# Performance work log

Hardware: AMD Instinct MI355X
Metric: run time of the kernel (lower is better)

Reference implementation:

```python
import jax, jax.numpy as jnp
import numpy as np

B, T, D = 32, 512, 1024   # batch, seq_len, input_dim
H, L, O = 1024, 4, 1024   # hidden_dim, num_layers, output_dim


def setup_inputs() -> dict:
    key = jax.random.key(0)
    ks = jax.random.split(key, 8)
    s_in = 1.0 / np.sqrt(D)
    s_h = 1.0 / np.sqrt(H)
    # Weights stored as [in, out]; y = x @ W + b (equivalent to torch Linear with W.T)
    return {
        "x":     jax.random.normal(ks[0], (B, T, D), dtype=jnp.float32),
        "W_in":  jax.random.uniform(ks[1], (L, D, H), minval=-s_in, maxval=s_in, dtype=jnp.float32),
        "b_in":  jax.random.uniform(ks[2], (L, H),    minval=-s_in, maxval=s_in, dtype=jnp.float32),
        "W_h":   jax.random.uniform(ks[3], (L, H, H), minval=-s_h,  maxval=s_h,  dtype=jnp.float32),
        "b_h":   jax.random.uniform(ks[4], (L, H),    minval=-s_h,  maxval=s_h,  dtype=jnp.float32),
        "tau":   jnp.ones((L, H), dtype=jnp.float32),
        "W_out": jax.random.uniform(ks[5], (H, O),    minval=-s_h,  maxval=s_h,  dtype=jnp.float32),
        "b_out": jax.random.uniform(ks[6], (O,),      minval=-s_h,  maxval=s_h,  dtype=jnp.float32),
    }


def reference(x, W_in, b_in, W_h, b_h, tau, W_out, b_out):
    n_layers = W_in.shape[0]

    def step(h, x_t):
        # h: [L, B, H]; x_t: [B, D]
        xt = x_t
        new_h = []
        for i in range(n_layers):
            dx = jnp.tanh(xt @ W_in[i] + b_in[i] + h[i] @ W_h[i] + b_h[i])
            hi = h[i] + (dx - h[i]) / tau[i]
            new_h.append(hi)
            xt = hi
        return jnp.stack(new_h), None

    h0 = jnp.zeros((n_layers, x.shape[0], W_h.shape[-1]), dtype=x.dtype)
    hT, _ = jax.lax.scan(step, h0, jnp.swapaxes(x, 0, 1))  # scan over time axis
    return hT[-1] @ W_out + b_out  # [B, O]
```

## Files before the change

### kernel.cpp

```cpp
#include <hip/hip_runtime.h>
#include <math.h>

#define B_ 32
#define T_ 512
#define D_ 1024
#define H_ 1024
#define L_ 4
#define NTICK (T_ + L_ - 1)
#define RPD 17
#define PACK_PER_BLK 32768

typedef unsigned long long u64;

__device__ __forceinline__ float4 load_state4(const float* p) {
    u64 a = __hip_atomic_load((const u64*)p,       __ATOMIC_RELAXED, __HIP_MEMORY_SCOPE_AGENT);
    u64 b = __hip_atomic_load((const u64*)(p + 2), __ATOMIC_RELAXED, __HIP_MEMORY_SCOPE_AGENT);
    float4 v;
    v.x = __uint_as_float((unsigned)(a & 0xffffffffu));
    v.y = __uint_as_float((unsigned)(a >> 32));
    v.z = __uint_as_float((unsigned)(b & 0xffffffffu));
    v.w = __uint_as_float((unsigned)(b >> 32));
    return v;
}

__device__ __forceinline__ void waitCount(const unsigned int* p, unsigned int target) {
    int c = 0;
    while (__hip_atomic_load(p, __ATOMIC_RELAXED, __HIP_MEMORY_SCOPE_AGENT) < target) {
        __builtin_amdgcn_s_sleep(16);
        if (++c > 20000) return;
    }
}

__global__ __launch_bounds__(512) void lnn_repack(
    const float* __restrict__ W_in, const float* __restrict__ W_h,
    float* __restrict__ Wpack)
{
    const int bid   = blockIdx.x;
    const int layer = bid >> 6;
    const int jbase = (bid & 63) << 4;
    const float* Win_l = W_in + (size_t)layer * D_ * H_;
    const float* Wh_l  = W_h  + (size_t)layer * H_ * H_;
    float* dst = Wpack + (size_t)bid * PACK_PER_BLK;
#pragma unroll 1
    for (int i = 0; i < 16; ++i) {
        const int f  = (i << 9) + threadIdx.x;
        const int d  = f << 2;
        const int jj = d >> 11;
        const int k  = d & 2047;
        const float* s = (k < 1024) ? &Win_l[(size_t)k * H_ + jbase + jj]
                                    : &Wh_l[(size_t)(k - 1024) * H_ + jbase + jj];
        float4 v;
        v.x = s[0];
        v.y = s[(size_t)H_];
        v.z = s[(size_t)2 * H_];
        v.w = s[(size_t)3 * H_];
        *(float4*)&dst[d] = v;
    }
}

#define REDUCE_PHASE(P)                                                         \
    do {                                                                        \
        __syncthreads();                                                        \
        _Pragma("unroll")                                                       \
        for (int q = 0; q < 8; ++q) {                                           \
            red[tid * RPD + (q << 1)]     = acc[((P) << 3) + q].x;              \
            red[tid * RPD + (q << 1) + 1] = acc[((P) << 3) + q].y;              \
        }                                                                       \
        __syncthreads();                                                        \
        if (tid < 128) {                                                        \
            const int bo   = tid >> 4;                                          \
            const int bh   = ((P) << 3) + bo;                                   \
            const int js   = (tid & 15) >> 1;                                   \
            const int comp = tid & 1;                                           \
            float s = 0.f;                                                      \
            _Pragma("unroll")                                                   \
            for (int ks = 0; ks < 64; ++ks)                                     \
                s += red[((ks << 3) + js) * RPD + (bo << 1) + comp];            \
            const float dx   = tanhf(s + bias);                                 \
            const float hold = __hip_atomic_load(&hrow[(size_t)bh * H_ + jr],   \
                                __ATOMIC_RELAXED, __HIP_MEMORY_SCOPE_AGENT);    \
            const float hn   = hold + (dx - hold) / tv;                         \
            __hip_atomic_store(&wl[(size_t)bh * H_ + jr], hn,                   \
                               __ATOMIC_RELAXED, __HIP_MEMORY_SCOPE_AGENT);     \
        }                                                                       \
    } while (0)

template<bool PACKED>
__global__ __launch_bounds__(512, 2) void lnn_persist(
    const float* __restrict__ x,
    const float* __restrict__ W_in,
    const float* __restrict__ b_in,
    const float* __restrict__ W_h,
    const float* __restrict__ b_h,
    const float* __restrict__ tau,
    const float* __restrict__ Wpack,
    float* __restrict__ buf0,
    float* __restrict__ buf1,
    unsigned int* __restrict__ count)
{
    const int tid   = threadIdx.x;
    const int layer = blockIdx.x >> 6;
    const int jbase = (blockIdx.x & 63) << 4;
    const int jp    = tid & 7;
    const int kslot = tid >> 3;
    const int kb    = kslot << 2;

    __shared__ __align__(16) float smem[16384];
    float (*xs)[32][256] = (float(*)[32][256])smem;
    float* red = smem;

    const float* Wl_in = W_in + (size_t)layer * D_ * H_;
    const float* Wl_h  = W_h  + (size_t)layer * H_ * H_;
    const float* wbaseA = Wpack + (size_t)blockIdx.x * PACK_PER_BLK
                        + ((size_t)(jp << 1) << 11);
    const float* wbaseB = wbaseA + 2048;
    const int jgA = jbase + (jp << 1);

    const int   jr   = jbase + (tid & 15);
    const float bias = b_in[layer * H_ + jr] + b_h[layer * H_ + jr];
    const float tv   = tau[layer * H_ + jr];

    const int srow = tid >> 6;
    const int scol = (tid & 63) << 2;

    for (int tick = 0; tick < NTICK; ++tick) {
        if (tid == 0 && tick > 0)
            waitCount(&count[tick - 1], 256u);
        __syncthreads();

        const int t = tick - layer;
        if (t >= 0 && t < T_) {
            const float* rb   = (tick & 1) ? buf0 : buf1;
            float*       wb   = (tick & 1) ? buf1 : buf0;
            const float* hrow = rb + (size_t)layer * B_ * H_;
            float*       wl   = wb + (size_t)layer * B_ * H_;

            const float* xsrc; size_t xstr;
            if (layer == 0) { xsrc = x + (size_t)t * D_;                  xstr = (size_t)T_ * D_; }
            else            { xsrc = rb + (size_t)(layer - 1) * B_ * H_;  xstr = H_; }

            float2 acc[32];
#pragma unroll
            for (int i = 0; i < 32; ++i) acc[i] = make_float2(0.f, 0.f);

            {
                const bool at0 = (layer != 0);
#pragma unroll
                for (int q = 0; q < 4; ++q) {
                    const int r = srow + (q << 3);
                    const float* sp = &xsrc[(size_t)r * xstr + scol];
                    float4 v = at0 ? load_state4(sp) : *(const float4*)sp;
                    *(float4*)&xs[0][r][scol] = v;
                }
            }
            __syncthreads();

#pragma unroll 1
            for (int tile = 0; tile < 8; ++tile) {
                const int cur = tile & 1;

                float4 wA, wB;
                if constexpr (PACKED) {
                    wA = *(const float4*)&wbaseA[(tile << 8) + kb];
                    wB = *(const float4*)&wbaseB[(tile << 8) + kb];
                } else {
                    const int kof = (tile & 3) << 8;
                    const float* wp = ((tile < 4) ? Wl_in : Wl_h)
                                    + (size_t)(kof + kb) * H_ + jgA;
                    wA.x = wp[0];            wB.x = wp[1];
                    wA.y = wp[(size_t)H_];   wB.y = wp[(size_t)H_ + 1];
                    wA.z = wp[2*(size_t)H_]; wB.z = wp[2*(size_t)H_ + 1];
                    wA.w = wp[3*(size_t)H_]; wB.w = wp[3*(size_t)H_ + 1];
                }

                float4 stg[4];
                if (tile < 7) {
                    const int    nt   = tile + 1;
                    const float* nsrc = (nt < 4) ? xsrc : hrow;
                    const size_t nstr = (nt < 4) ? xstr : (size_t)H_;
                    const int    nkof = (nt & 3) << 8;
                    const bool   nat  = (nt >= 4) || (layer != 0);
#pragma unroll
                    for (int q = 0; q < 4; ++q) {
                        const int r = srow + (q << 3);
                        const float* sp = &nsrc[(size_t)r * nstr + nkof + scol];
                        stg[q] = nat ? load_state4(sp) : *(const float4*)sp;
                    }
                }

#pragma unroll
                for (int b = 0; b < 32; ++b) {
                    const float4 a = *(const float4*)&xs[cur][b][kb];
                    acc[b].x += a.x * wA.x + a.y * wA.y + a.z * wA.z + a.w * wA.w;
                    acc[b].y += a.x * wB.x + a.y * wB.y + a.z * wB.z + a.w * wB.w;
                }

                if (tile < 7) {
#pragma unroll
                    for (int q = 0; q < 4; ++q)
                        *(float4*)&xs[cur ^ 1][srow + (q << 3)][scol] = stg[q];
                }
                __syncthreads();
            }

            REDUCE_PHASE(0); REDUCE_PHASE(1); REDUCE_PHASE(2); REDUCE_PHASE(3);
        }

        __syncthreads();
        if (tid == 0)
            __hip_atomic_fetch_add(&count[tick], 1u,
                                   __ATOMIC_RELEASE, __HIP_MEMORY_SCOPE_AGENT);
    }
}

__global__ __launch_bounds__(256) void lnn_out(
    const float* __restrict__ H3,
    const float* __restrict__ W_out,
    const float* __restrict__ b_out,
    float* __restrict__ out)
{
    const int gid = blockIdx.x * 256 + threadIdx.x;
    const int jj  = gid & 1023;
    const int b2  = gid >> 10;
    float acc0 = b_out[jj];
    float acc1 = b_out[jj];
    for (int k = 0; k < H_; ++k) {
        const float w = W_out[k * H_ + jj];
        acc0 += H3[b2 * H_ + k]        * w;
        acc1 += H3[(b2 + 16) * H_ + k] * w;
    }
    out[b2 * H_ + jj]        = acc0;
    out[(b2 + 16) * H_ + jj] = acc1;
}

extern "C" void kernel_launch(void* const* d_in, const int* in_sizes, int n_in,
                              void* d_out, int out_size, void* d_ws, size_t ws_size,
                              hipStream_t stream) {
    const float* x     = (const float*)d_in[0];
    const float* W_in  = (const float*)d_in[1];
    const float* b_in  = (const float*)d_in[2];
    const float* W_h   = (const float*)d_in[3];
    const float* b_h   = (const float*)d_in[4];
    const float* tau   = (const float*)d_in[5];
    const float* W_out = (const float*)d_in[6];
    const float* b_out = (const float*)d_in[7];

    const size_t stateElems = (size_t)L_ * B_ * H_;
    const size_t packElems  = (size_t)256 * PACK_PER_BLK;
    const size_t needPacked = (packElems + 2 * stateElems) * sizeof(float)
                            + NTICK * sizeof(unsigned int);
    const bool packed = (ws_size >= needPacked);

    float* Wpack = (float*)d_ws;
    float* buf0  = packed ? (Wpack + packElems) : (float*)d_ws;
    float* buf1  = buf0 + stateElems;
    unsigned int* count = (unsigned int*)(buf1 + stateElems);

    (void)hipMemsetAsync(buf0, 0,
                         2 * stateElems * sizeof(float) + NTICK * sizeof(unsigned int), stream);

    if (packed) {
        lnn_repack<<<256, 512, 0, stream>>>(W_in, W_h, Wpack);
        lnn_persist<true><<<256, 512, 0, stream>>>(x, W_in, b_in, W_h, b_h, tau,
                                                   Wpack, buf0, buf1, count);
    } else {
        lnn_persist<false><<<256, 512, 0, stream>>>(x, W_in, b_in, W_h, b_h, tau,
                                                    Wpack, buf0, buf1, count);
    }

    const float* H3 = buf0 + 3 * (B_ * H_);
    lnn_out<<<64, 256, 0, stream>>>(H3, W_out, b_out, (float*)d_out);
}
```

Baseline: 15.54 ms.

## Shard tick counters and stage two K-tiles per barrier in persistent RNN

The single per-tick arrival counter becomes 8 padded sub-counters. Each block increments the one chosen by its block index, and the waiter sums all 8, so the 256 atomic adds no longer hit one address. Shared memory doubles to hold two 256-wide K-tiles per buffer half, so the inner loop handles tiles in pairs and issues half as many __syncthreads per timestep. The trade-offs are 128KB of LDS per block, which rules out the two-blocks-per-CU occupancy the launch bounds ask for, and a waiter that must poll 8 cache lines per tick.

Result: no change. 15.71 ms (+1.1%).

```diff
diff --git a/kernel.cpp b/kernel.cpp
--- a/kernel.cpp
+++ b/kernel.cpp
@@ -9,6 +9,8 @@
 #define NTICK (T_ + L_ - 1)
 #define RPD 17
 #define PACK_PER_BLK 32768
+#define CNT_STRIDE 16
+#define CNT_PER_TICK (8 * CNT_STRIDE)
 
 typedef unsigned long long u64;
 
@@ -23,9 +25,15 @@
     return v;
 }
 
-__device__ __forceinline__ void waitCount(const unsigned int* p, unsigned int target) {
+__device__ __forceinline__ void waitTick(const unsigned int* base) {
     int c = 0;
-    while (__hip_atomic_load(p, __ATOMIC_RELAXED, __HIP_MEMORY_SCOPE_AGENT) < target) {
+    for (;;) {
+        unsigned s = 0;
+#pragma unroll
+        for (int i = 0; i < 8; ++i)
+            s += __hip_atomic_load(base + i * CNT_STRIDE,
+                                   __ATOMIC_RELAXED, __HIP_MEMORY_SCOPE_AGENT);
+        if (s >= 256u) return;
         __builtin_amdgcn_s_sleep(16);
         if (++c > 20000) return;
     }
@@ -85,6 +93,25 @@
         }                                                                       \
     } while (0)
 
+#define STAGE_TILE(TSRC, TSTR, TKOF, TAT, DSTPTR)                               \
+    do {                                                                        \
+        float4 stg0, stg1, stg2, stg3;                                          \
+        {                                                                       \
+            const float* sp0 = &(TSRC)[(size_t)(srow)      * (TSTR) + (TKOF) + scol]; \
+            const float* sp1 = &(TSRC)[(size_t)(srow + 8)  * (TSTR) + (TKOF) + scol]; \
+            const float* sp2 = &(TSRC)[(size_t)(srow + 16) * (TSTR) + (TKOF) + scol]; \
+            const float* sp3 = &(TSRC)[(size_t)(srow + 24) * (TSTR) + (TKOF) + scol]; \
+            if (TAT) { stg0 = load_state4(sp0); stg1 = load_state4(sp1);        \
+                       stg2 = load_state4(sp2); stg3 = load_state4(sp3); }      \
+            else     { stg0 = *(const float4*)sp0; stg1 = *(const float4*)sp1;  \
+                       stg2 = *(const float4*)sp2; stg3 = *(const float4*)sp3; }\
+        }                                                                       \
+        *(float4*)&(DSTPTR)[(size_t)(srow)      * 256 + scol] = stg0;           \
+        *(float4*)&(DSTPTR)[(size_t)(srow + 8)  * 256 + scol] = stg1;           \
+        *(float4*)&(DSTPTR)[(size_t)(srow + 16) * 256 + scol] = stg2;           \
+        *(float4*)&(DSTPTR)[(size_t)(srow + 24) * 256 + scol] = stg3;           \
+    } while (0)
+
 template<bool PACKED>
 __global__ __launch_bounds__(512, 2) void lnn_persist(
     const float* __restrict__ x,
@@ -105,8 +132,7 @@
     const int kslot = tid >> 3;
     const int kb    = kslot << 2;
 
-    __shared__ __align__(16) float smem[16384];
-    float (*xs)[32][256] = (float(*)[32][256])smem;
+    __shared__ __align__(16) float smem[32768];
     float* red = smem;
 
     const float* Wl_in = W_in + (size_t)layer * D_ * H_;
@@ -125,7 +151,7 @@
 
     for (int tick = 0; tick < NTICK; ++tick) {
         if (tid == 0 && tick > 0)
-            waitCount(&count[tick - 1], 256u);
+            waitTick(count + (size_t)(tick - 1) * CNT_PER_TICK);
         __syncthreads();
 
         const int t = tick - layer;
@@ -138,68 +164,83 @@
             const float* xsrc; size_t xstr;
             if (layer == 0) { xsrc = x + (size_t)t * D_;                  xstr = (size_t)T_ * D_; }
             else            { xsrc = rb + (size_t)(layer - 1) * B_ * H_;  xstr = H_; }
+            const bool xat = (layer != 0);
 
             float2 acc[32];
 #pragma unroll
             for (int i = 0; i < 32; ++i) acc[i] = make_float2(0.f, 0.f);
 
-            {
-                const bool at0 = (layer != 0);
+            STAGE_TILE(xsrc, xstr, 0,   xat, smem);
+            STAGE_TILE(xsrc, xstr, 256, xat, smem + 8192);
+            __syncthreads();
+
+#pragma unroll 1
+            for (int p = 0; p < 4; ++p) {
+                const int    bufo = (p & 1) << 14;
+                const int    nbo  = ((p & 1) ^ 1) << 14;
+                const float* cs0  = smem + bufo;
+                const float* cs1  = smem + bufo + 8192;
+                const int ta = (p << 1);
+                const int tb = ta + 1;
+
+                {
+                    float4 wA, wB;
+                    if constexpr (PACKED) {
+                        wA = *(const float4*)&wbaseA[(ta << 8) + kb];
+                        wB = *(const float4*)&wbaseB[(ta << 8) + kb];
+                    } else {
+                        const float* wp = ((ta < 4) ? Wl_in : Wl_h)
+                                        + (size_t)(((ta & 3) << 8) + kb) * H_ + jgA;
+                        wA.x = wp[0];            wB.x = wp[1];
+                        wA.y = wp[(size_t)H_];   wB.y = wp[(size_t)H_ + 1];
+                        wA.z = wp[2*(size_t)H_]; wB.z = wp[2*(size_t)H_ + 1];
+                        wA.w = wp[3*(size_t)H_]; wB.w = wp[3*(size_t)H_ + 1];
+                    }
+                    if (p < 3) {
+                        const int    nt   = ta + 2;
+                        const float* nsrc = (nt < 4) ? xsrc : hrow;
+                        const size_t nstr = (nt < 4) ? xstr : (size_t)H_;
+                        const int    nkof = (nt & 3) << 8;
+                        const bool   nat  = (nt >= 4) || xat;
+                        STAGE_TILE(nsrc, nstr, nkof, nat, smem + nbo);
+                    }
 #pragma unroll
-                for (int q = 0; q < 4; ++q) {
-                    const int r = srow + (q << 3);
-                    const float* sp = &xsrc[(size_t)r * xstr + scol];
-                    float4 v = at0 ? load_state4(sp) : *(const float4*)sp;
-                    *(float4*)&xs[0][r][scol] = v;
+                    for (int b = 0; b < 32; ++b) {
+                        const float4 a = *(const float4*)&cs0[(size_t)b * 256 + kb];
+                        acc[b].x += a.x * wA.x + a.y * wA.y + a.z * wA.z + a.w * wA.w;
+                        acc[b].y += a.x * wB.x + a.y * wB.y + a.z * wB.z + a.w * wB.w;
+                    }
                 }
-            }
-            __syncthreads();
-
-#pragma unroll 1
-            for (int tile = 0; tile < 8; ++tile) {
-                const int cur = tile & 1;
-
-                float4 wA, wB;
-                if constexpr (PACKED) {
-                    wA = *(const float4*)&wbaseA[(tile << 8) + kb];
-                    wB = *(const float4*)&wbaseB[(tile << 8) + kb];
-                } else {
-                    const int kof = (tile & 3) << 8;
-                    const float* wp = ((tile < 4) ? Wl_in : Wl_h)
-                                    + (size_t)(kof + kb) * H_ + jgA;
-                    wA.x = wp[0];            wB.x = wp[1];
-                    wA.y = wp[(size_t)H_];   wB.y = wp[(size_t)H_ + 1];
-                    wA.z = wp[2*(size_t)H_]; wB.z = wp[2*(size_t)H_ + 1];
-                    wA.w = wp[3*(size_t)H_]; wB.w = wp[3*(size_t)H_ + 1];
+
+                {
+                    float4 wA, wB;
+                    if constexpr (PACKED) {
+                        wA = *(const float4*)&wbaseA[(tb << 8) + kb];
+                        wB = *(const float4*)&wbaseB[(tb << 8) + kb];
+                    } else {
+                        const float* wp = ((tb < 4) ? Wl_in : Wl_h)
+                                        + (size_t)(((tb & 3) << 8) + kb) * H_ + jgA;
+                        wA.x = wp[0];            wB.x = wp[1];
+                        wA.y = wp[(size_t)H_];   wB.y = wp[(size_t)H_ + 1];
+                        wA.z = wp[2*(size_t)H_]; wB.z = wp[2*(size_t)H_ + 1];
+                        wA.w = wp[3*(size_t)H_]; wB.w = wp[3*(size_t)H_ + 1];
+                    }
+                    if (p < 3) {
+                        const int    nt   = tb + 2;
+                        const float* nsrc = (nt < 4) ? xsrc : hrow;
+                        const size_t nstr = (nt < 4) ? xstr : (size_t)H_;
+                        const int    nkof = (nt & 3) << 8;
+                        const bool   nat  = (nt >= 4) || xat;
+                        STAGE_TILE(nsrc, nstr, nkof, nat, smem + nbo + 8192);
+                    }
+#pragma unroll
+                    for (int b = 0; b < 32; ++b) {
+                        const float4 a = *(const float4*)&cs1[(size_t)b * 256 + kb];
+                        acc[b].x += a.x * wA.x + a.y * wA.y + a.z * wA.z + a.w * wA.w;
+                        acc[b].y += a.x * wB.x + a.y * wB.y + a.z * wB.z + a.w * wB.w;
+                    }
                 }
 
-                float4 stg[4];
-                if (tile < 7) {
-                    const int    nt   = tile + 1;
-                    const float* nsrc = (nt < 4) ? xsrc : hrow;
-                    const size_t nstr = (nt < 4) ? xstr : (size_t)H_;
-                    const int    nkof = (nt & 3) << 8;
-                    const bool   nat  = (nt >= 4) || (layer != 0);
-#pragma unroll
-                    for (int q = 0; q < 4; ++q) {
-                        const int r = srow + (q << 3);
-                        const float* sp = &nsrc[(size_t)r * nstr + nkof + scol];
-                        stg[q] = nat ? load_state4(sp) : *(const float4*)sp;
-                    }
-                }
-
-#pragma unroll
-                for (int b = 0; b < 32; ++b) {
-                    const float4 a = *(const float4*)&xs[cur][b][kb];
-                    acc[b].x += a.x * wA.x + a.y * wA.y + a.z * wA.z + a.w * wA.w;
-                    acc[b].y += a.x * wB.x + a.y * wB.y + a.z * wB.z + a.w * wB.w;
-                }
-
-                if (tile < 7) {
-#pragma unroll
-                    for (int q = 0; q < 4; ++q)
-                        *(float4*)&xs[cur ^ 1][srow + (q << 3)][scol] = stg[q];
-                }
                 __syncthreads();
             }
 
@@ -208,7 +249,8 @@
 
         __syncthreads();
         if (tid == 0)
-            __hip_atomic_fetch_add(&count[tick], 1u,
+            __hip_atomic_fetch_add(count + (size_t)tick * CNT_PER_TICK
+                                         + (blockIdx.x & 7) * CNT_STRIDE, 1u,
                                    __ATOMIC_RELEASE, __HIP_MEMORY_SCOPE_AGENT);
     }
 }
@@ -247,8 +289,9 @@
 
     const size_t stateElems = (size_t)L_ * B_ * H_;
     const size_t packElems  = (size_t)256 * PACK_PER_BLK;
+    const size_t cntDwords  = (size_t)NTICK * CNT_PER_TICK;
     const size_t needPacked = (packElems + 2 * stateElems) * sizeof(float)
-                            + NTICK * sizeof(unsigned int);
+                            + cntDwords * sizeof(unsigned int);
     const bool packed = (ws_size >= needPacked);
 
     float* Wpack = (float*)d_ws;
@@ -257,7 +300,8 @@
     unsigned int* count = (unsigned int*)(buf1 + stateElems);
 
     (void)hipMemsetAsync(buf0, 0,
-                         2 * stateElems * sizeof(float) + NTICK * sizeof(unsigned int), stream);
+                         2 * stateElems * sizeof(float) + cntDwords * sizeof(unsigned int),
+                         stream);
 
     if (packed) {
         lnn_repack<<<256, 512, 0, stream>>>(W_in, W_h, Wpack);
```

## Replace global per-tick barrier with per-layer dataflow dependency counters

Applied to the files above, without the earlier changes.

Instead of all 256 blocks waiting on a single global counter per tick, each layer's blocks now wait only on their true dependencies: the previous layer at the same timestep, their own layer at the previous timestep, and the next layer two steps back (to protect the double buffer against WAR). This lets layers advance independently as a wavefront and removes the idle tick at the pipeline ends. It adds up to three waits per step and a larger counter array.

Result: faster. 13.31 ms (median of 2 runs) (-14.4%).

```diff
diff --git a/kernel.cpp b/kernel.cpp
--- a/kernel.cpp
+++ b/kernel.cpp
@@ -6,7 +6,6 @@
 #define D_ 1024
 #define H_ 1024
 #define L_ 4
-#define NTICK (T_ + L_ - 1)
 #define RPD 17
 #define PACK_PER_BLK 32768
 
@@ -96,7 +95,7 @@
     const float* __restrict__ Wpack,
     float* __restrict__ buf0,
     float* __restrict__ buf1,
-    unsigned int* __restrict__ count)
+    unsigned int* __restrict__ done)
 {
     const int tid   = threadIdx.x;
     const int layer = blockIdx.x >> 6;
@@ -123,92 +122,93 @@
     const int srow = tid >> 6;
     const int scol = (tid & 63) << 2;
 
-    for (int tick = 0; tick < NTICK; ++tick) {
-        if (tid == 0 && tick > 0)
-            waitCount(&count[tick - 1], 256u);
+    for (int t = 0; t < T_; ++t) {
+        if (tid == 0) {
+            if (layer > 0)             waitCount(&done[(layer - 1) * T_ + t],     64u);
+            if (t >= 1)                waitCount(&done[layer * T_ + (t - 1)],     64u);
+            if (layer < 3 && t >= 2)   waitCount(&done[(layer + 1) * T_ + (t - 2)], 64u);
+        }
         __syncthreads();
 
-        const int t = tick - layer;
-        if (t >= 0 && t < T_) {
-            const float* rb   = (tick & 1) ? buf0 : buf1;
-            float*       wb   = (tick & 1) ? buf1 : buf0;
-            const float* hrow = rb + (size_t)layer * B_ * H_;
-            float*       wl   = wb + (size_t)layer * B_ * H_;
-
-            const float* xsrc; size_t xstr;
-            if (layer == 0) { xsrc = x + (size_t)t * D_;                  xstr = (size_t)T_ * D_; }
-            else            { xsrc = rb + (size_t)(layer - 1) * B_ * H_;  xstr = H_; }
-
-            float2 acc[32];
-#pragma unroll
-            for (int i = 0; i < 32; ++i) acc[i] = make_float2(0.f, 0.f);
-
-            {
-                const bool at0 = (layer != 0);
+        const int par = (t + layer) & 1;
+        const float* rb   = par ? buf0 : buf1;
+        float*       wb   = par ? buf1 : buf0;
+        const float* hrow = rb + (size_t)layer * B_ * H_;
+        float*       wl   = wb + (size_t)layer * B_ * H_;
+
+        const float* xsrc; size_t xstr;
+        if (layer == 0) { xsrc = x + (size_t)t * D_;                  xstr = (size_t)T_ * D_; }
+        else            { xsrc = rb + (size_t)(layer - 1) * B_ * H_;  xstr = H_; }
+
+        float2 acc[32];
+#pragma unroll
+        for (int i = 0; i < 32; ++i) acc[i] = make_float2(0.f, 0.f);
+
+        {
+            const bool at0 = (layer != 0);
+#pragma unroll
+            for (int q = 0; q < 4; ++q) {
+                const int r = srow + (q << 3);
+                const float* sp = &xsrc[(size_t)r * xstr + scol];
+                float4 v = at0 ? load_state4(sp) : *(const float4*)sp;
+                *(float4*)&xs[0][r][scol] = v;
+            }
+        }
+        __syncthreads();
+
+#pragma unroll 1
+        for (int tile = 0; tile < 8; ++tile) {
+            const int cur = tile & 1;
+
+            float4 wA, wB;
+            if constexpr (PACKED) {
+                wA = *(const float4*)&wbaseA[(tile << 8) + kb];
+                wB = *(const float4*)&wbaseB[(tile << 8) + kb];
+            } else {
+                const int kof = (tile & 3) << 8;
+                const float* wp = ((tile < 4) ? Wl_in : Wl_h)
+                                + (size_t)(kof + kb) * H_ + jgA;
+                wA.x = wp[0];            wB.x = wp[1];
+                wA.y = wp[(size_t)H_];   wB.y = wp[(size_t)H_ + 1];
+                wA.z = wp[2*(size_t)H_]; wB.z = wp[2*(size_t)H_ + 1];
+                wA.w = wp[3*(size_t)H_]; wB.w = wp[3*(size_t)H_ + 1];
+            }
+
+            float4 stg[4];
+            if (tile < 7) {
+                const int    nt   = tile + 1;
+                const float* nsrc = (nt < 4) ? xsrc : hrow;
+                const size_t nstr = (nt < 4) ? xstr : (size_t)H_;
+                const int    nkof = (nt & 3) << 8;
+                const bool   nat  = (nt >= 4) || (layer != 0);
 #pragma unroll
                 for (int q = 0; q < 4; ++q) {
                     const int r = srow + (q << 3);
-                    const float* sp = &xsrc[(size_t)r * xstr + scol];
-                    float4 v = at0 ? load_state4(sp) : *(const float4*)sp;
-                    *(float4*)&xs[0][r][scol] = v;
+                    const float* sp = &nsrc[(size_t)r * nstr + nkof + scol];
+                    stg[q] = nat ? load_state4(sp) : *(const float4*)sp;
                 }
             }
+
+#pragma unroll
+            for (int b = 0; b < 32; ++b) {
+                const float4 a = *(const float4*)&xs[cur][b][kb];
+                acc[b].x += a.x * wA.x + a.y * wA.y + a.z * wA.z + a.w * wA.w;
+                acc[b].y += a.x * wB.x + a.y * wB.y + a.z * wB.z + a.w * wB.w;
+            }
+
+            if (tile < 7) {
+#pragma unroll
+                for (int q = 0; q < 4; ++q)
+                    *(float4*)&xs[cur ^ 1][srow + (q << 3)][scol] = stg[q];
+            }
             __syncthreads();
-
-#pragma unroll 1
-            for (int tile = 0; tile < 8; ++tile) {
-                const int cur = tile & 1;
-
-                float4 wA, wB;
-                if constexpr (PACKED) {
-                    wA = *(const float4*)&wbaseA[(tile << 8) + kb];
-                    wB = *(const float4*)&wbaseB[(tile << 8) + kb];
-                } else {
-                    const int kof = (tile & 3) << 8;
-                    const float* wp = ((tile < 4) ? Wl_in : Wl_h)
-                                    + (size_t)(kof + kb) * H_ + jgA;
-                    wA.x = wp[0];            wB.x = wp[1];
-                    wA.y = wp[(size_t)H_];   wB.y = wp[(size_t)H_ + 1];
-                    wA.z = wp[2*(size_t)H_]; wB.z = wp[2*(size_t)H_ + 1];
-                    wA.w = wp[3*(size_t)H_]; wB.w = wp[3*(size_t)H_ + 1];
-                }
-
-                float4 stg[4];
-                if (tile < 7) {
-                    const int    nt   = tile + 1;
-                    const float* nsrc = (nt < 4) ? xsrc : hrow;
-                    const size_t nstr = (nt < 4) ? xstr : (size_t)H_;
-                    const int    nkof = (nt & 3) << 8;
-                    const bool   nat  = (nt >= 4) || (layer != 0);
-#pragma unroll
-                    for (int q = 0; q < 4; ++q) {
-                        const int r = srow + (q << 3);
-                        const float* sp = &nsrc[(size_t)r * nstr + nkof + scol];
-                        stg[q] = nat ? load_state4(sp) : *(const float4*)sp;
-                    }
-                }
-
-#pragma unroll
-                for (int b = 0; b < 32; ++b) {
-                    const float4 a = *(const float4*)&xs[cur][b][kb];
-                    acc[b].x += a.x * wA.x + a.y * wA.y + a.z * wA.z + a.w * wA.w;
-                    acc[b].y += a.x * wB.x + a.y * wB.y + a.z * wB.z + a.w * wB.w;
-                }
-
-                if (tile < 7) {
-#pragma unroll
-                    for (int q = 0; q < 4; ++q)
-                        *(float4*)&xs[cur ^ 1][srow + (q << 3)][scol] = stg[q];
-                }
-                __syncthreads();
-            }
-
-            REDUCE_PHASE(0); REDUCE_PHASE(1); REDUCE_PHASE(2); REDUCE_PHASE(3);
         }
+
+        REDUCE_PHASE(0); REDUCE_PHASE(1); REDUCE_PHASE(2); REDUCE_PHASE(3);
 
         __syncthreads();
         if (tid == 0)
-            __hip_atomic_fetch_add(&count[tick], 1u,
+            __hip_atomic_fetch_add(&done[layer * T_ + t], 1u,
                                    __ATOMIC_RELEASE, __HIP_MEMORY_SCOPE_AGENT);
     }
 }
@@ -247,25 +247,27 @@
 
     const size_t stateElems = (size_t)L_ * B_ * H_;
     const size_t packElems  = (size_t)256 * PACK_PER_BLK;
+    const size_t cntDwords  = (size_t)L_ * T_;
     const size_t needPacked = (packElems + 2 * stateElems) * sizeof(float)
-                            + NTICK * sizeof(unsigned int);
+                            + cntDwords * sizeof(unsigned int);
     const bool packed = (ws_size >= needPacked);
 
     float* Wpack = (float*)d_ws;
     float* buf0  = packed ? (Wpack + packElems) : (float*)d_ws;
     float* buf1  = buf0 + stateElems;
-    unsigned int* count = (unsigned int*)(buf1 + stateElems);
+    unsigned int* done = (unsigned int*)(buf1 + stateElems);
 
     (void)hipMemsetAsync(buf0, 0,
-                         2 * stateElems * sizeof(float) + NTICK * sizeof(unsigned int), stream);
+                         2 * stateElems * sizeof(float) + cntDwords * sizeof(unsigned int),
+                         stream);
 
     if (packed) {
         lnn_repack<<<256, 512, 0, stream>>>(W_in, W_h, Wpack);
         lnn_persist<true><<<256, 512, 0, stream>>>(x, W_in, b_in, W_h, b_h, tau,
-                                                   Wpack, buf0, buf1, count);
+                                                   Wpack, buf0, buf1, done);
     } else {
         lnn_persist<false><<<256, 512, 0, stream>>>(x, W_in, b_in, W_h, b_h, tau,
-                                                    Wpack, buf0, buf1, count);
+                                                    Wpack, buf0, buf1, done);
     }
 
     const float* H3 = buf0 + 3 * (B_ * H_);
```
